# Performance work log

Hardware: AMD Instinct MI355X
Metric: run time of the kernel (lower is better)

Reference implementation:

```python
import jax, jax.numpy as jnp
import numpy as np

B, S, D, H = 8, 1024, 1024, 16
DH = D // H


def setup_inputs() -> dict:
    key = jax.random.key(0)
    ks = jax.random.split(key, 7)
    scale = 1.0 / np.sqrt(DH)
    return {
        "sequences": jax.random.normal(ks[0], (B, S, D), dtype=jnp.float32),
        "Wq": jax.random.uniform(ks[1], (H, DH, DH), jnp.float32, -scale, scale),
        "bq": jax.random.uniform(ks[2], (H, DH), jnp.float32, -scale, scale),
        "Wk": jax.random.uniform(ks[3], (H, DH, DH), jnp.float32, -scale, scale),
        "bk": jax.random.uniform(ks[4], (H, DH), jnp.float32, -scale, scale),
        "Wv": jax.random.uniform(ks[5], (H, DH, DH), jnp.float32, -scale, scale),
        "bv": jax.random.uniform(ks[6], (H, DH), jnp.float32, -scale, scale),
    }


def reference(sequences, Wq, bq, Wk, bk, Wv, bv):
    # split channels into heads: [B,S,H,DH]
    x = sequences.reshape(B, S, H, DH)
    # per-head linear maps (torch Linear: y = x @ W.T + b)
    q = jnp.einsum("bshd,hed->bshe", x, Wq) + bq  # [B,S,H,DH]
    k = jnp.einsum("bshd,hed->bshe", x, Wk) + bk
    v = jnp.einsum("bshd,hed->bshe", x, Wv) + bv
    scores = jnp.einsum("bshd,bthd->bhst", q, k) / jnp.sqrt(jnp.asarray(DH, x.dtype))
    attn = jax.nn.softmax(scores, axis=-1)  # [B,H,S,S]
    out = jnp.einsum("bhst,bthd->bshd", attn, v)  # [B,S,H,DH]
    return out.reshape(B, S, D)
```

## Files before the change

### kernel.cpp

```cpp
#include <hip/hip_runtime.h>
#include <hip/hip_bf16.h>


constexpr int NB = 8, NS = 1024, ND = 1024, NH = 16, NDH = 64;

typedef __bf16 bf16x8 __attribute__((ext_vector_type(8)));
typedef float f32x4 __attribute__((ext_vector_type(4)));

__device__ __forceinline__ f32x4 mfma16(bf16x8 a, bf16x8 b, f32x4 c) {
  return __builtin_amdgcn_mfma_f32_16x16x32_bf16(a, b, c, 0, 0, 0);
}

__device__ __forceinline__ float fast_exp2(float x) {
#if __has_builtin(__builtin_amdgcn_exp2f)
  return __builtin_amdgcn_exp2f(x);
#else
  return __builtin_exp2f(x);
#endif
}

__device__ __forceinline__ bf16x8 cvt2bf8(float4 lo, float4 hi) {
  bf16x8 r;
  r[0] = (__bf16)lo.x; r[1] = (__bf16)lo.y; r[2] = (__bf16)lo.z; r[3] = (__bf16)lo.w;
  r[4] = (__bf16)hi.x; r[5] = (__bf16)hi.y; r[6] = (__bf16)hi.z; r[7] = (__bf16)hi.w;
  return r;
}

__device__ __forceinline__ void gload16(const __hip_bfloat16* g, __hip_bfloat16* l) {
  __builtin_amdgcn_global_load_lds(
      (const __attribute__((address_space(1))) void*)g,
      (__attribute__((address_space(3))) void*)l, 16, 0, 0);
}

__device__ __forceinline__ unsigned pack_bf16(float hi, float lo) {
  unsigned uh = __builtin_bit_cast(unsigned, hi) + 0x8000u;
  unsigned ul = __builtin_bit_cast(unsigned, lo) + 0x8000u;
  return __builtin_amdgcn_perm(uh, ul, 0x07060302u);
}

__global__ __launch_bounds__(256) void qkv_proj_kernel(
    const float* __restrict__ x,
    const float* __restrict__ Wq, const float* __restrict__ bq,
    const float* __restrict__ Wk, const float* __restrict__ bk,
    const float* __restrict__ Wv, const float* __restrict__ bv,
    __hip_bfloat16* __restrict__ Qo, __hip_bfloat16* __restrict__ Ko,
    __hip_bfloat16* __restrict__ Vt) {
  __shared__ __align__(16) __hip_bfloat16 Wlds[3][NDH][72];
  const int tid = threadIdx.x;
  const int wave = tid >> 6, lane = tid & 63;
  const int m = lane & 15, quad = lane >> 4;
  const int h = blockIdx.x & (NH - 1);
  const int sblk = blockIdx.x >> 4;

  const float* Ws[3] = {Wq + h * 4096, Wk + h * 4096, Wv + h * 4096};
#pragma unroll
  for (int mt = 0; mt < 3; mt++) {
#pragma unroll
    for (int p = 0; p < 4; p++) {
      int idx = (p * 256 + tid) * 4;
      float4 v = *(const float4*)(Ws[mt] + idx);
      __align__(8) __hip_bfloat16 t4[4] = {
          __float2bfloat16(v.x), __float2bfloat16(v.y),
          __float2bfloat16(v.z), __float2bfloat16(v.w)};
      *(uint2*)&Wlds[mt][idx >> 6][idx & 63] = *(const uint2*)t4;
    }
  }
  __syncthreads();

  float bq4[4][4], bk4[4][4], bvv[4];
#pragma unroll
  for (int nt = 0; nt < 4; nt++) {
    float4 a = *(const float4*)(bq + h * 64 + nt * 16 + quad * 4);
    float4 c = *(const float4*)(bk + h * 64 + nt * 16 + quad * 4);
    bq4[nt][0] = a.x; bq4[nt][1] = a.y; bq4[nt][2] = a.z; bq4[nt][3] = a.w;
    bk4[nt][0] = c.x; bk4[nt][1] = c.y; bk4[nt][2] = c.z; bk4[nt][3] = c.w;
    bvv[nt] = bv[h * 64 + nt * 16 + m];
  }

  const int rowbase = sblk * 256 + wave * 64;
  bf16x8 Xf[4][2];
#pragma unroll
  for (int st = 0; st < 4; st++) {
    const float* xp = x + (size_t)(rowbase + st * 16 + m) * ND + h * NDH + quad * 8;
#pragma unroll
    for (int c = 0; c < 2; c++) {
      float4 lo = *(const float4*)(xp + c * 32);
      float4 hi = *(const float4*)(xp + c * 32 + 4);
      Xf[st][c] = cvt2bf8(lo, hi);
    }
  }

  const int b = rowbase >> 10;
  const int s0 = rowbase & 1023;
  const float qscale = 0.18033688011112042f;

#pragma unroll
  for (int mt = 0; mt < 3; mt++) {
#pragma unroll
    for (int nt = 0; nt < 4; nt++) {
      bf16x8 w0 = *(const bf16x8*)&Wlds[mt][nt * 16 + m][quad * 8];
      bf16x8 w1 = *(const bf16x8*)&Wlds[mt][nt * 16 + m][32 + quad * 8];
#pragma unroll
      for (int st = 0; st < 4; st++) {
        f32x4 acc = {0.f, 0.f, 0.f, 0.f};
        if (mt < 2) {
          acc = mfma16(w0, Xf[st][0], acc);
          acc = mfma16(w1, Xf[st][1], acc);
          const int srow = s0 + st * 16 + m;
          __align__(8) __hip_bfloat16 t4[4];
          if (mt == 0) {
#pragma unroll
            for (int r = 0; r < 4; r++)
              t4[r] = __float2bfloat16((acc[r] + bq4[nt][r]) * qscale);
            *(uint2*)(Qo + ((size_t)(b * NH + h) * NS + srow) * NDH +
                      nt * 16 + quad * 4) = *(const uint2*)t4;
          } else {
#pragma unroll
            for (int r = 0; r < 4; r++)
              t4[r] = __float2bfloat16(acc[r] + bk4[nt][r]);
            *(uint2*)(Ko + ((size_t)(b * NH + h) * NS + srow) * NDH +
                      nt * 16 + quad * 4) = *(const uint2*)t4;
          }
        } else {
          acc = mfma16(Xf[st][0], w0, acc);
          acc = mfma16(Xf[st][1], w1, acc);
          __align__(8) __hip_bfloat16 t4[4];
#pragma unroll
          for (int r = 0; r < 4; r++) t4[r] = __float2bfloat16(acc[r] + bvv[nt]);
          *(uint2*)(Vt + ((size_t)(b * NH + h) * NDH + nt * 16 + m) * NS + s0 +
                    st * 16 + quad * 4) = *(const uint2*)t4;
        }
      }
    }
  }
}

__global__ __launch_bounds__(256, 2) void attn_kernel(
    const __hip_bfloat16* __restrict__ Q,
    const __hip_bfloat16* __restrict__ K,
    const __hip_bfloat16* __restrict__ Vt,
    float* __restrict__ out) {
  __shared__ __align__(16) __hip_bfloat16 Kt[2][64][64];
  __shared__ __align__(16) __hip_bfloat16 Vl[2][64][64];

  const int tid = threadIdx.x;
  const int wave = tid >> 6, lane = tid & 63;
  const int m = lane & 15, quad = lane >> 4;

  const int xcd = blockIdx.x & 7;
  const int j = blockIdx.x >> 3;
  const int bh = xcd * 16 + (j & 15);
  const int qblk = j >> 4;
  const int qbase = qblk * 256 + wave * 64;

  const __hip_bfloat16* Qp = Q + (size_t)bh * NS * NDH;
  const __hip_bfloat16* Kp = K + (size_t)bh * NS * NDH;
  const __hip_bfloat16* Vp = Vt + (size_t)bh * NDH * NS;

  bf16x8 Bq[4][2];
#pragma unroll
  for (int g = 0; g < 4; g++)
#pragma unroll
    for (int dh = 0; dh < 2; dh++)
      Bq[g][dh] = *(const bf16x8*)(Qp + (size_t)(qbase + g * 16 + m) * NDH +
                                   dh * 32 + quad * 8);

  f32x4 accO[4][4];
  f32x4 lsum[4];
#pragma unroll
  for (int g = 0; g < 4; g++) {
    lsum[g] = (f32x4){0.f, 0.f, 0.f, 0.f};
#pragma unroll
    for (int nt = 0; nt < 4; nt++) accO[g][nt] = (f32x4){0.f, 0.f, 0.f, 0.f};
  }
  bf16x8 ones8;
#pragma unroll
  for (int i = 0; i < 8; i++) ones8[i] = (__bf16)1.0f;

  const int r8 = lane >> 3;
  const int csV = (lane & 7) ^ r8;
  const int csK0 = (lane & 7) ^ (r8 & 3);
  const int krow = 8 * (m >> 2) + (m & 3);
  const int fK = (m & 3) ^ (((m >> 2) & 1) << 2);
  const int kc0 = ((quad ^ fK)) * 8;
  const int vc0 = ((quad ^ (m & 7))) * 8;

#define STAGE(buf, tb)                                                        \
  {                                                                           \
    _Pragma("unroll") for (int p8 = 0; p8 < 2; p8++) {                        \
      const int row0 = wave * 16 + p8 * 8;                                    \
      gload16(Kp + (size_t)((tb) * 64 + row0 + r8) * NDH +                    \
                  (csK0 ^ (p8 * 4)) * 8,                                      \
              &Kt[buf][row0][0]);                                             \
      gload16(Vp + (size_t)(row0 + r8) * NS + (tb) * 64 + csV * 8,            \
              &Vl[buf][row0][0]);                                             \
    }                                                                         \
  }

  STAGE(0, 0);

  for (int tb = 0; tb < NS / 64; tb++) {
    const int cur = tb & 1;
    __syncthreads();
    if (tb + 1 < NS / 64) STAGE(cur ^ 1, tb + 1);

    bf16x8 Pa[4][2];
#pragma unroll
    for (int c = 0; c < 2; c++) {
      uint2 pw[4][2];
#pragma unroll
      for (int p = 0; p < 2; p++) {
        const __hip_bfloat16* kr = &Kt[cur][c * 32 + 4 * p + krow][0];
        bf16x8 k0 = *(const bf16x8*)(kr + kc0);
        bf16x8 k1 = *(const bf16x8*)(kr + (kc0 ^ 32));
#pragma unroll
        for (int g = 0; g < 4; g++) {
          f32x4 a = {0.f, 0.f, 0.f, 0.f};
          a = mfma16(k0, Bq[g][0], a);
          a = mfma16(k1, Bq[g][1], a);
          pw[g][p].x = pack_bf16(fast_exp2(a[1]), fast_exp2(a[0]));
          pw[g][p].y = pack_bf16(fast_exp2(a[3]), fast_exp2(a[2]));
        }
      }
#pragma unroll
      for (int g = 0; g < 4; g++) {
        uint4 u = {pw[g][0].x, pw[g][0].y, pw[g][1].x, pw[g][1].y};
        Pa[g][c] = __builtin_bit_cast(bf16x8, u);
      }
    }
#pragma unroll
    for (int g = 0; g < 4; g++)
#pragma unroll
      for (int c = 0; c < 2; c++) lsum[g] = mfma16(Pa[g][c], ones8, lsum[g]);
#pragma unroll
    for (int nt = 0; nt < 4; nt++) {
      const __hip_bfloat16* vr = &Vl[cur][nt * 16 + m][0];
      bf16x8 v0 = *(const bf16x8*)(vr + vc0);
      bf16x8 v1 = *(const bf16x8*)(vr + (vc0 ^ 32));
#pragma unroll
      for (int g = 0; g < 4; g++) {
        accO[g][nt] = mfma16(Pa[g][0], v0, accO[g][nt]);
        accO[g][nt] = mfma16(Pa[g][1], v1, accO[g][nt]);
      }
    }
  }
#undef STAGE

  const int b = bh >> 4, h = bh & (NH - 1);
#pragma unroll
  for (int g = 0; g < 4; g++) {
#pragma unroll
    for (int r = 0; r < 4; r++) {
      float inv = 1.0f / lsum[g][r];
      int srow = qbase + g * 16 + quad * 4 + r;
      float* op = out + (size_t)(b * NS + srow) * ND + h * NDH;
#pragma unroll
      for (int nt = 0; nt < 4; nt++) op[nt * 16 + m] = accO[g][nt][r] * inv;
    }
  }
}

extern "C" void kernel_launch(void* const* d_in, const int* in_sizes, int n_in,
                              void* d_out, int out_size, void* d_ws, size_t ws_size,
                              hipStream_t stream) {
  const float* x  = (const float*)d_in[0];
  const float* Wq = (const float*)d_in[1];
  const float* bq = (const float*)d_in[2];
  const float* Wk = (const float*)d_in[3];
  const float* bk = (const float*)d_in[4];
  const float* Wv = (const float*)d_in[5];
  const float* bv = (const float*)d_in[6];
  float* out = (float*)d_out;

  const size_t elems = (size_t)NB * NH * NS * NDH;
  __hip_bfloat16* Qw = (__hip_bfloat16*)d_ws;
  __hip_bfloat16* Kw = Qw + elems;
  __hip_bfloat16* Vw = Kw + elems;

  qkv_proj_kernel<<<512, 256, 0, stream>>>(x, Wq, bq, Wk, bk, Wv, bv, Qw, Kw, Vw);
  attn_kernel<<<512, 256, 0, stream>>>(Qw, Kw, Vw, out);
}
```

Measured before the change: 145.7 us.

## Software-pipeline attention loop: overlap QK/exp of next tile with PV of previous

Restructures the attention main loop so that S=QK^T and exp2 for tile i are interleaved with the P·V MFMAs and row-sum updates for tile i-1. V gets a triple-buffered shared-memory ring so the previous tile's V stays live while the next one is staged. The aim is to hide the transcendental exp and pack work behind matrix-core work within a wave. The cost is more live registers (two score sets plus previous and current P), which risks spills under the 256x2 launch bound, and extra LDS for the third V buffer.

```diff
diff --git a/kernel.cpp b/kernel.cpp
--- a/kernel.cpp
+++ b/kernel.cpp
@@ -141,7 +141,7 @@
     const __hip_bfloat16* __restrict__ Vt,
     float* __restrict__ out) {
   __shared__ __align__(16) __hip_bfloat16 Kt[2][64][64];
-  __shared__ __align__(16) __hip_bfloat16 Vl[2][64][64];
+  __shared__ __align__(16) __hip_bfloat16 Vl[3][64][64];
 
   const int tid = threadIdx.x;
   const int wave = tid >> 6, lane = tid & 63;
@@ -182,69 +182,113 @@
   const int csK0 = (lane & 7) ^ (r8 & 3);
   const int krow = 8 * (m >> 2) + (m & 3);
   const int fK = (m & 3) ^ (((m >> 2) & 1) << 2);
-  const int kc0 = ((quad ^ fK)) * 8;
-  const int vc0 = ((quad ^ (m & 7))) * 8;
-
-#define STAGE(buf, tb)                                                        \
+  const int kc0 = (quad ^ fK) * 8;
+  const int vc0 = (quad ^ (m & 7)) * 8;
+
+#define STAGE_K(buf, tb)                                                      \
   {                                                                           \
     _Pragma("unroll") for (int p8 = 0; p8 < 2; p8++) {                        \
       const int row0 = wave * 16 + p8 * 8;                                    \
       gload16(Kp + (size_t)((tb) * 64 + row0 + r8) * NDH +                    \
                   (csK0 ^ (p8 * 4)) * 8,                                      \
               &Kt[buf][row0][0]);                                             \
+    }                                                                         \
+  }
+#define STAGE_V(buf, tb)                                                      \
+  {                                                                           \
+    _Pragma("unroll") for (int p8 = 0; p8 < 2; p8++) {                        \
+      const int row0 = wave * 16 + p8 * 8;                                    \
       gload16(Vp + (size_t)(row0 + r8) * NS + (tb) * 64 + csV * 8,            \
               &Vl[buf][row0][0]);                                             \
     }                                                                         \
   }
 
-  STAGE(0, 0);
-
-  for (int tb = 0; tb < NS / 64; tb++) {
-    const int cur = tb & 1;
+#define QK_CHUNK(kb, c, a)                                                    \
+  {                                                                           \
+    _Pragma("unroll") for (int p = 0; p < 2; p++) {                           \
+      const __hip_bfloat16* kr = &Kt[kb][(c) * 32 + 4 * p + krow][0];         \
+      bf16x8 k0 = *(const bf16x8*)(kr + kc0);                                 \
+      bf16x8 k1 = *(const bf16x8*)(kr + (kc0 ^ 32));                          \
+      _Pragma("unroll") for (int g = 0; g < 4; g++) {                         \
+        f32x4 t = {0.f, 0.f, 0.f, 0.f};                                       \
+        t = mfma16(k0, Bq[g][0], t);                                          \
+        a[g][p] = mfma16(k1, Bq[g][1], t);                                    \
+      }                                                                       \
+    }                                                                         \
+  }
+#define EXP_CHUNK(c, a, P)                                                    \
+  {                                                                           \
+    _Pragma("unroll") for (int g = 0; g < 4; g++) {                           \
+      uint4 u;                                                                \
+      u.x = pack_bf16(fast_exp2(a[g][0][1]), fast_exp2(a[g][0][0]));          \
+      u.y = pack_bf16(fast_exp2(a[g][0][3]), fast_exp2(a[g][0][2]));          \
+      u.z = pack_bf16(fast_exp2(a[g][1][1]), fast_exp2(a[g][1][0]));          \
+      u.w = pack_bf16(fast_exp2(a[g][1][3]), fast_exp2(a[g][1][2]));          \
+      P[g][c] = __builtin_bit_cast(bf16x8, u);                                \
+    }                                                                         \
+  }
+#define PV_HALF(vb, nt0, P)                                                   \
+  {                                                                           \
+    _Pragma("unroll") for (int nt = (nt0); nt < (nt0) + 2; nt++) {            \
+      const __hip_bfloat16* vr = &Vl[vb][nt * 16 + m][0];                     \
+      bf16x8 v0 = *(const bf16x8*)(vr + vc0);                                 \
+      bf16x8 v1 = *(const bf16x8*)(vr + (vc0 ^ 32));                          \
+      _Pragma("unroll") for (int g = 0; g < 4; g++) {                         \
+        accO[g][nt] = mfma16(P[g][0], v0, accO[g][nt]);                       \
+        accO[g][nt] = mfma16(P[g][1], v1, accO[g][nt]);                       \
+      }                                                                       \
+    }                                                                         \
+  }
+
+  STAGE_K(0, 0); STAGE_V(0, 0);
+  __syncthreads();
+  STAGE_K(1, 1); STAGE_V(1, 1);
+
+  bf16x8 Pp[4][2];
+  {
+    f32x4 a[4][2];
+    QK_CHUNK(0, 0, a); EXP_CHUNK(0, a, Pp);
+    QK_CHUNK(0, 1, a); EXP_CHUNK(1, a, Pp);
+  }
+
+  for (int i = 1; i < 16; i++) {
+    const int kb = i & 1;
+    const int vb = (i - 1) % 3;
     __syncthreads();
-    if (tb + 1 < NS / 64) STAGE(cur ^ 1, tb + 1);
-
-    bf16x8 Pa[4][2];
-#pragma unroll
-    for (int c = 0; c < 2; c++) {
-      uint2 pw[4][2];
-#pragma unroll
-      for (int p = 0; p < 2; p++) {
-        const __hip_bfloat16* kr = &Kt[cur][c * 32 + 4 * p + krow][0];
-        bf16x8 k0 = *(const bf16x8*)(kr + kc0);
-        bf16x8 k1 = *(const bf16x8*)(kr + (kc0 ^ 32));
-#pragma unroll
-        for (int g = 0; g < 4; g++) {
-          f32x4 a = {0.f, 0.f, 0.f, 0.f};
-          a = mfma16(k0, Bq[g][0], a);
-          a = mfma16(k1, Bq[g][1], a);
-          pw[g][p].x = pack_bf16(fast_exp2(a[1]), fast_exp2(a[0]));
-          pw[g][p].y = pack_bf16(fast_exp2(a[3]), fast_exp2(a[2]));
-        }
-      }
-#pragma unroll
-      for (int g = 0; g < 4; g++) {
-        uint4 u = {pw[g][0].x, pw[g][0].y, pw[g][1].x, pw[g][1].y};
-        Pa[g][c] = __builtin_bit_cast(bf16x8, u);
-      }
-    }
-#pragma unroll
-    for (int g = 0; g < 4; g++)
-#pragma unroll
-      for (int c = 0; c < 2; c++) lsum[g] = mfma16(Pa[g][c], ones8, lsum[g]);
-#pragma unroll
-    for (int nt = 0; nt < 4; nt++) {
-      const __hip_bfloat16* vr = &Vl[cur][nt * 16 + m][0];
-      bf16x8 v0 = *(const bf16x8*)(vr + vc0);
-      bf16x8 v1 = *(const bf16x8*)(vr + (vc0 ^ 32));
-#pragma unroll
-      for (int g = 0; g < 4; g++) {
-        accO[g][nt] = mfma16(Pa[g][0], v0, accO[g][nt]);
-        accO[g][nt] = mfma16(Pa[g][1], v1, accO[g][nt]);
-      }
-    }
-  }
-#undef STAGE
+    if (i < 15) { STAGE_K((i + 1) & 1, i + 1); STAGE_V((i + 1) % 3, i + 1); }
+
+    bf16x8 Pc[4][2];
+    f32x4 a0[4][2], a1[4][2];
+    QK_CHUNK(kb, 0, a0);
+#pragma unroll
+    for (int g = 0; g < 4; g++) {
+      lsum[g] = mfma16(Pp[g][0], ones8, lsum[g]);
+      lsum[g] = mfma16(Pp[g][1], ones8, lsum[g]);
+    }
+    PV_HALF(vb, 0, Pp);
+    EXP_CHUNK(0, a0, Pc);
+    QK_CHUNK(kb, 1, a1);
+    PV_HALF(vb, 2, Pp);
+    EXP_CHUNK(1, a1, Pc);
+#pragma unroll
+    for (int g = 0; g < 4; g++) {
+      Pp[g][0] = Pc[g][0];
+      Pp[g][1] = Pc[g][1];
+    }
+  }
+#pragma unroll
+  for (int g = 0; g < 4; g++) {
+    lsum[g] = mfma16(Pp[g][0], ones8, lsum[g]);
+    lsum[g] = mfma16(Pp[g][1], ones8, lsum[g]);
+  }
+  PV_HALF(0, 0, Pp);
+  PV_HALF(0, 2, Pp);
+
+#undef STAGE_K
+#undef STAGE_V
+#undef QK_CHUNK
+#undef EXP_CHUNK
+#undef PV_HALF
 
   const int b = bh >> 4, h = bh & (NH - 1);
 #pragma unroll
```

After: 145.7 us. About the same (+0.1%).
